# Optimization experiments

Hardware: AMD Instinct MI355X
Metric: run time of the kernel (lower is better)

## Reference

```python
import jax, jax.numpy as jnp
import numpy as np

N, K, C = 128, 64, 64

def _w(key, shape, scale):
    return (jax.random.normal(key, shape, dtype=jnp.float32) * scale)

def setup_inputs() -> dict:
    key = jax.random.key(0)
    ks = jax.random.split(key, 20)
    s1 = 1.0 / np.sqrt(C)
    s2 = 1.0 / np.sqrt(2 * C)
    inp = {
        "x": jax.random.normal(ks[0], (N, K, C), dtype=jnp.float32),
        "W_lin": _w(ks[1], (C, C), s1), "b_lin": jnp.zeros((C,), jnp.float32),
        # unary_passing: Linear(C,C) -> tanh -> Linear(C,C)
        "Wu1": _w(ks[2], (C, C), s1), "bu1": jnp.zeros((C,), jnp.float32),
        "Wu2": _w(ks[3], (C, C), s1), "bu2": jnp.zeros((C,), jnp.float32),
        # unary_gate: Linear(C,C) -> tanh -> Linear(C,C) -> sigmoid
        "Wug1": _w(ks[4], (C, C), s1), "bug1": jnp.zeros((C,), jnp.float32),
        "Wug2": _w(ks[5], (C, C), s1), "bug2": jnp.zeros((C,), jnp.float32),
        # binary_passing: Linear(2C,C) -> tanh -> Linear(C,C)
        "Wb1": _w(ks[6], (2 * C, C), s2), "bb1": jnp.zeros((C,), jnp.float32),
        "Wb2": _w(ks[7], (C, C), s1), "bb2": jnp.zeros((C,), jnp.float32),
        # binary_gate: Linear(2C,C) -> tanh -> Linear(C,C) -> sigmoid
        "Wbg1": _w(ks[8], (2 * C, C), s2), "bbg1": jnp.zeros((C,), jnp.float32),
        "Wbg2": _w(ks[9], (C, C), s1), "bbg2": jnp.zeros((C,), jnp.float32),
        "t": 0,  # time scalar, ignored by IgnoreLinear base layer
    }
    return inp


def reference(x, W_lin, b_lin, Wu1, bu1, Wu2, bu2, Wug1, bug1, Wug2, bug2,
              Wb1, bb1, Wb2, bb2, Wbg1, bbg1, Wbg2, bbg2, t):
    # base linear map (IgnoreLinear: ignores t)
    h = x @ W_lin + b_lin                          # (N, K, C)
    n, k, c = h.shape
    # unary message with gate
    um = jnp.tanh(h @ Wu1 + bu1) @ Wu2 + bu2
    ug = jax.nn.sigmoid(jnp.tanh(h @ Wug1 + bug1) @ Wug2 + bug2)
    um = um * ug                                   # (N, K, C)
    # all-pairs broadcast-concat: hm[n,i,j] = [h[n,j], h[n,i]]
    hm = jnp.concatenate([
        jnp.broadcast_to(h[:, None, :, :], (n, k, k, c)),
        jnp.broadcast_to(h[:, :, None, :], (n, k, k, c)),
    ], axis=3)                                     # (N, K, K, 2C)
    bm = jnp.tanh(hm @ Wb1 + bb1) @ Wb2 + bb2      # (N, K, K, C)
    bg = jax.nn.sigmoid(jnp.tanh(hm @ Wbg1 + bbg1) @ Wbg2 + bbg2)
    # sum over axis 1 (includes diagonal, as in original), normalize by K-1
    bm = jnp.sum(bm * bg, axis=1) / jnp.float32(k - 1)  # (N, K, C)
    return um + bm
```

## Files before the change

### kernel.cpp

```cpp
#include <hip/hip_runtime.h>

#define WST 72

typedef __attribute__((ext_vector_type(4))) float    f32x4;
typedef __attribute__((ext_vector_type(2))) float    f32x2;
typedef __attribute__((ext_vector_type(8))) _Float16 f16x8;
typedef __attribute__((ext_vector_type(2))) _Float16 f16x2;

__device__ __forceinline__ float rcp_f(float x) { return __builtin_amdgcn_rcpf(x); }
__device__ __forceinline__ float fast_sigmoid(float x) {
    return rcp_f(1.0f + __expf(-x));
}
__device__ __forceinline__ float tanh_exp(float x) {
    return 1.0f - 2.0f * rcp_f(__expf(2.0f * x) + 1.0f);
}

__device__ __forceinline__ void stage512(const float* __restrict__ W,
                                         _Float16* Wt, int tid) {
#pragma unroll
    for (int i = 0; i < 8; ++i) {
        int idx = tid + i * 512;
        int k = idx >> 6, c = idx & 63;
        Wt[c * WST + k] = (_Float16)W[idx];
    }
}

__device__ __forceinline__ void gemm2(const _Float16* Act, int arow, int qd,
                                      const _Float16* Wt, int colb,
                                      f32x4 acc[2]) {
    f16x8 a0 = *(const f16x8*)(Act + arow * WST + qd * 8);
    f16x8 a1 = *(const f16x8*)(Act + arow * WST + 32 + qd * 8);
#pragma unroll
    for (int cc = 0; cc < 2; ++cc) {
        const _Float16* wr = Wt + (colb + cc * 16) * WST + qd * 8;
        f16x8 b0 = *(const f16x8*)(wr);
        f16x8 b1 = *(const f16x8*)(wr + 32);
        acc[cc] = __builtin_amdgcn_mfma_f32_16x16x32_f16(a0, b0, acc[cc], 0, 0, 0);
        acc[cc] = __builtin_amdgcn_mfma_f32_16x16x32_f16(a1, b1, acc[cc], 0, 0, 0);
    }
}

__global__ __launch_bounds__(512, 2) void fused_all_kernel(
    const float* __restrict__ x,
    const float* __restrict__ W_lin, const float* __restrict__ b_lin,
    const float* __restrict__ Wu1,  const float* __restrict__ bu1,
    const float* __restrict__ Wu2,  const float* __restrict__ bu2,
    const float* __restrict__ Wug1, const float* __restrict__ bug1,
    const float* __restrict__ Wug2, const float* __restrict__ bug2,
    const float* __restrict__ Wb1,  const float* __restrict__ bb1,
    const float* __restrict__ Wb2,  const float* __restrict__ bb2,
    const float* __restrict__ Wbg1, const float* __restrict__ bbg1,
    const float* __restrict__ Wbg2, const float* __restrict__ bbg2,
    float* __restrict__ out)
{
    __shared__ __align__(16) char smem[113664];
    _Float16* Wt0  = (_Float16*)(smem);
    _Float16* Wt1  = (_Float16*)(smem + 9216);
    _Float16* Ax   = (_Float16*)(smem + 18432);
    _Float16* Ah   = (_Float16*)(smem + 27648);
    _Float16* Au   = (_Float16*)(smem + 36864);
    _Float16* Agg  = (_Float16*)(smem + 46080);
    float*    EQb  = (float*)(smem + 55296);
    float*    EQgb = (float*)(smem + 71680);
    float*    EPm  = (float*)(smem + 88064);
    float*    EPgm = (float*)(smem + 96768);
    float*    um32 = (float*)(smem + 105472);
    float*    Red  = (float*)(smem);

    int tid = threadIdx.x, w = tid >> 6, l = tid & 63;
    int qd = l >> 4, l16 = l & 15;
    int n = blockIdx.x >> 1, jsel = blockIdx.x & 1;

    int rw = w & 3, ch = w >> 2;
    int arow = rw * 16 + l16;
    int colb = ch * 32 + l16;
    int crow = rw * 16 + qd * 4;
    bool mine = (rw >> 1) == jsel;
    int lr0 = (rw & 1) * 16 + qd * 4;

    f32x4 acc[2];

#pragma unroll
    for (int i = 0; i < 4; ++i) {
        int e = tid * 2 + i * 1024;
        f32x2 v = *(const f32x2*)(x + (size_t)n * 4096 + e);
        f16x2 p; p[0] = (_Float16)v[0]; p[1] = (_Float16)v[1];
        *(f16x2*)(Ax + (e >> 6) * WST + (e & 63)) = p;
    }
    stage512(W_lin, Wt0, tid);
    __syncthreads();

#pragma unroll
    for (int cc = 0; cc < 2; ++cc) {
        float bv = b_lin[colb + cc * 16];
        acc[cc] = (f32x4){bv, bv, bv, bv};
    }
    gemm2(Ax, arow, qd, Wt0, colb, acc);
#pragma unroll
    for (int cc = 0; cc < 2; ++cc)
#pragma unroll
        for (int r = 0; r < 4; ++r)
            Ah[(crow + r) * WST + colb + cc * 16] = (_Float16)acc[cc][r];
    stage512(Wb1, Wt1, tid);
    __syncthreads();

#pragma unroll
    for (int cc = 0; cc < 2; ++cc) {
        float bv = bb1[colb + cc * 16];
        acc[cc] = (f32x4){bv, bv, bv, bv};
    }
    gemm2(Ah, arow, qd, Wt1, colb, acc);
    if (mine) {
#pragma unroll
        for (int cc = 0; cc < 2; ++cc)
#pragma unroll
            for (int r = 0; r < 4; ++r)
                EPm[(lr0 + r) * 68 + colb + cc * 16] = __expf(2.0f * acc[cc][r]);
    }
    stage512(Wb1 + 4096, Wt0, tid);
    __syncthreads();

    acc[0] = (f32x4){0.f, 0.f, 0.f, 0.f};
    acc[1] = (f32x4){0.f, 0.f, 0.f, 0.f};
    gemm2(Ah, arow, qd, Wt0, colb, acc);
#pragma unroll
    for (int cc = 0; cc < 2; ++cc)
#pragma unroll
        for (int r = 0; r < 4; ++r)
            EQb[(crow + r) * 64 + colb + cc * 16] = __expf(2.0f * acc[cc][r]);
    stage512(Wbg1, Wt1, tid);
    __syncthreads();

#pragma unroll
    for (int cc = 0; cc < 2; ++cc) {
        float bv = bbg1[colb + cc * 16];
        acc[cc] = (f32x4){bv, bv, bv, bv};
    }
    gemm2(Ah, arow, qd, Wt1, colb, acc);
    if (mine) {
#pragma unroll
        for (int cc = 0; cc < 2; ++cc)
#pragma unroll
            for (int r = 0; r < 4; ++r)
                EPgm[(lr0 + r) * 68 + colb + cc * 16] = __expf(2.0f * acc[cc][r]);
    }
    stage512(Wbg1 + 4096, Wt0, tid);
    __syncthreads();

    acc[0] = (f32x4){0.f, 0.f, 0.f, 0.f};
    acc[1] = (f32x4){0.f, 0.f, 0.f, 0.f};
    gemm2(Ah, arow, qd, Wt0, colb, acc);
#pragma unroll
    for (int cc = 0; cc < 2; ++cc)
#pragma unroll
        for (int r = 0; r < 4; ++r)
            EQgb[(crow + r) * 64 + colb + cc * 16] = __expf(2.0f * acc[cc][r]);
    stage512(Wu1, Wt1, tid);
    __syncthreads();

#pragma unroll
    for (int cc = 0; cc < 2; ++cc) {
        float bv = bu1[colb + cc * 16];
        acc[cc] = (f32x4){bv, bv, bv, bv};
    }
    gemm2(Ah, arow, qd, Wt1, colb, acc);
#pragma unroll
    for (int cc = 0; cc < 2; ++cc)
#pragma unroll
        for (int r = 0; r < 4; ++r)
            Au[(crow + r) * WST + colb + cc * 16] = (_Float16)tanh_exp(acc[cc][r]);
    stage512(Wug1, Wt0, tid);
    __syncthreads();

#pragma unroll
    for (int cc = 0; cc < 2; ++cc) {
        float bv = bug1[colb + cc * 16];
        acc[cc] = (f32x4){bv, bv, bv, bv};
    }
    gemm2(Ah, arow, qd, Wt0, colb, acc);
#pragma unroll
    for (int cc = 0; cc < 2; ++cc)
#pragma unroll
        for (int r = 0; r < 4; ++r)
            Agg[(crow + r) * WST + colb + cc * 16] = (_Float16)tanh_exp(acc[cc][r]);
    stage512(Wu2, Wt1, tid);
    __syncthreads();

    f32x4 uacc[2];
#pragma unroll
    for (int cc = 0; cc < 2; ++cc) {
        float bv = bu2[colb + cc * 16];
        uacc[cc] = (f32x4){bv, bv, bv, bv};
    }
    gemm2(Au, arow, qd, Wt1, colb, uacc);
    stage512(Wug2, Wt0, tid);
    __syncthreads();

#pragma unroll
    for (int cc = 0; cc < 2; ++cc) {
        float bv = bug2[colb + cc * 16];
        acc[cc] = (f32x4){bv, bv, bv, bv};
    }
    gemm2(Agg, arow, qd, Wt0, colb, acc);
    if (mine) {
#pragma unroll
        for (int cc = 0; cc < 2; ++cc)
#pragma unroll
            for (int r = 0; r < 4; ++r)
                um32[(lr0 + r) * 64 + colb + cc * 16] =
                    uacc[cc][r] * fast_sigmoid(acc[cc][r]);
    }
    stage512(Wb2, Wt1, tid);
    stage512(Wbg2, Au, tid);
    __syncthreads();

    int jgrp = w >> 2, iw = w & 3;

    f16x8 bwm[4][2], bwg[4][2];
#pragma unroll
    for (int cc = 0; cc < 4; ++cc)
#pragma unroll
        for (int kk = 0; kk < 2; ++kk) {
            bwm[cc][kk] = *(const f16x8*)(Wt1 + (cc * 16 + l16) * WST + kk * 32 + qd * 8);
            bwg[cc][kk] = *(const f16x8*)(Au  + (cc * 16 + l16) * WST + kk * 32 + qd * 8);
        }
    float bim[4], big[4];
#pragma unroll
    for (int cc = 0; cc < 4; ++cc) {
        bim[cc] = bb2[cc * 16 + l16];
        big[cc] = bbg2[cc * 16 + l16];
    }

    const float* pr  = EPm  + (jgrp * 16 + l16) * 68;
    const float* pgr = EPgm + (jgrp * 16 + l16) * 68;
    f32x4 pm[4], pg[4];
    pm[0] = *(const f32x4*)(pr + qd * 8);
    pm[1] = *(const f32x4*)(pr + qd * 8 + 4);
    pm[2] = *(const f32x4*)(pr + 32 + qd * 8);
    pm[3] = *(const f32x4*)(pr + 32 + qd * 8 + 4);
    pg[0] = *(const f32x4*)(pgr + qd * 8);
    pg[1] = *(const f32x4*)(pgr + qd * 8 + 4);
    pg[2] = *(const f32x4*)(pgr + 32 + qd * 8);
    pg[3] = *(const f32x4*)(pgr + 32 + qd * 8 + 4);

    f32x4 bacc[4];
#pragma unroll
    for (int cc = 0; cc < 4; ++cc) bacc[cc] = (f32x4){0.f, 0.f, 0.f, 0.f};

    for (int ii = iw * 16; ii < iw * 16 + 16; ++ii) {
        const float* qm = EQb  + ii * 64;
        const float* qg = EQgb + ii * 64;
        f16x8 am[2], ag[2];
#pragma unroll
        for (int kk = 0; kk < 2; ++kk) {
            int cb = kk * 32 + qd * 8;
            f32x4 qa = *(const f32x4*)(qm + cb);
            f32x4 qb = *(const f32x4*)(qm + cb + 4);
            f32x4 ha = *(const f32x4*)(qg + cb);
            f32x4 hb = *(const f32x4*)(qg + cb + 4);
#pragma unroll
            for (int t = 0; t < 4; ++t) {
                am[kk][t]     = (_Float16)(1.0f - 2.0f * rcp_f(__builtin_fmaf(pm[kk*2][t],   qa[t], 1.0f)));
                am[kk][t + 4] = (_Float16)(1.0f - 2.0f * rcp_f(__builtin_fmaf(pm[kk*2+1][t], qb[t], 1.0f)));
                ag[kk][t]     = (_Float16)(1.0f - 2.0f * rcp_f(__builtin_fmaf(pg[kk*2][t],   ha[t], 1.0f)));
                ag[kk][t + 4] = (_Float16)(1.0f - 2.0f * rcp_f(__builtin_fmaf(pg[kk*2+1][t], hb[t], 1.0f)));
            }
        }
#pragma unroll
        for (int cc = 0; cc < 4; ++cc) {
            f32x4 d = {bim[cc], bim[cc], bim[cc], bim[cc]};
            d = __builtin_amdgcn_mfma_f32_16x16x32_f16(am[0], bwm[cc][0], d, 0, 0, 0);
            d = __builtin_amdgcn_mfma_f32_16x16x32_f16(am[1], bwm[cc][1], d, 0, 0, 0);
            f32x4 e = {big[cc], big[cc], big[cc], big[cc]};
            e = __builtin_amdgcn_mfma_f32_16x16x32_f16(ag[0], bwg[cc][0], e, 0, 0, 0);
            e = __builtin_amdgcn_mfma_f32_16x16x32_f16(ag[1], bwg[cc][1], e, 0, 0, 0);
#pragma unroll
            for (int r = 0; r < 4; ++r)
                bacc[cc][r] += d[r] * fast_sigmoid(e[r]);
        }
    }

    __syncthreads();
#pragma unroll
    for (int cc = 0; cc < 4; ++cc)
#pragma unroll
        for (int r = 0; r < 4; ++r)
            Red[(jgrp * 4 + iw) * 1024 + (qd * 4 + r) * 64 + cc * 16 + l16] = bacc[cc][r];
    __syncthreads();

    {
        int e = tid * 4;
        int lr = e >> 6, col = e & 63;
        int g = lr >> 4, rr = lr & 15;
        f32x4 s = {0.f, 0.f, 0.f, 0.f};
#pragma unroll
        for (int w2 = 0; w2 < 4; ++w2)
            s += *(const f32x4*)(Red + (g * 4 + w2) * 1024 + rr * 64 + col);
        f32x4 u = *(const f32x4*)(um32 + lr * 64 + col);
        f32x4 o;
#pragma unroll
        for (int t = 0; t < 4; ++t)
            o[t] = u[t] + s[t] * (1.0f / 63.0f);
        *(f32x4*)(out + (size_t)n * 4096 + (size_t)(jsel * 32 + lr) * 64 + col) = o;
    }
}

extern "C" void kernel_launch(void* const* d_in, const int* in_sizes, int n_in,
                              void* d_out, int out_size, void* d_ws, size_t ws_size,
                              hipStream_t stream)
{
    (void)in_sizes; (void)n_in; (void)out_size; (void)d_ws; (void)ws_size;
    const float* x     = (const float*)d_in[0];
    const float* W_lin = (const float*)d_in[1];
    const float* b_lin = (const float*)d_in[2];
    const float* Wu1   = (const float*)d_in[3];
    const float* bu1   = (const float*)d_in[4];
    const float* Wu2   = (const float*)d_in[5];
    const float* bu2   = (const float*)d_in[6];
    const float* Wug1  = (const float*)d_in[7];
    const float* bug1  = (const float*)d_in[8];
    const float* Wug2  = (const float*)d_in[9];
    const float* bug2  = (const float*)d_in[10];
    const float* Wb1   = (const float*)d_in[11];
    const float* bb1   = (const float*)d_in[12];
    const float* Wb2   = (const float*)d_in[13];
    const float* bb2   = (const float*)d_in[14];
    const float* Wbg1  = (const float*)d_in[15];
    const float* bbg1  = (const float*)d_in[16];
    const float* Wbg2  = (const float*)d_in[17];
    const float* bbg2  = (const float*)d_in[18];

    hipLaunchKernelGGL(fused_all_kernel, dim3(256), dim3(512), 0, stream,
        x, W_lin, b_lin, Wu1, bu1, Wu2, bu2, Wug1, bug1, Wug2, bug2,
        Wb1, bb1, Wb2, bb2, Wbg1, bbg1, Wbg2, bbg2,
        (float*)d_out);
}
```

Baseline: 118.7 us.

## Split each batch into four blocks, fold tanh/sigmoid constants into weights

The grid doubles to four blocks per batch element, each producing 16 output rows. Shared memory drops to about 78 KB and launch bounds now allow 4 blocks per CU, aiming for higher occupancy and more parallelism. The tanh affine terms are folded into the second-layer weights and biases by scaling W by -2 and 2*log2e and using column sums, so the inner loop computes reciprocals without the 1-2x step and uses exp2. Paired reciprocals, packed RTZ half conversion, and per-iteration LDS weight loads replace register-held weights. In exchange, the small prologue GEMMs are recomputed across the four blocks, and fp16 rounding of the scaled weights may shift accuracy slightly.

```diff
diff --git a/kernel.cpp b/kernel.cpp
--- a/kernel.cpp
+++ b/kernel.cpp
@@ -1,28 +1,43 @@
 #include <hip/hip_runtime.h>
 
 #define WST 72
+#define LOG2E 1.44269504f
 
 typedef __attribute__((ext_vector_type(4))) float    f32x4;
 typedef __attribute__((ext_vector_type(2))) float    f32x2;
 typedef __attribute__((ext_vector_type(8))) _Float16 f16x8;
 typedef __attribute__((ext_vector_type(2))) _Float16 f16x2;
+typedef __attribute__((ext_vector_type(2))) __fp16   fp16x2_raw;
+
+union U8 { f16x8 v; f16x2 h[4]; };
 
 __device__ __forceinline__ float rcp_f(float x) { return __builtin_amdgcn_rcpf(x); }
+__device__ __forceinline__ float exp2_f(float x) { return __builtin_amdgcn_exp2f(x); }
 __device__ __forceinline__ float fast_sigmoid(float x) {
     return rcp_f(1.0f + __expf(-x));
 }
 __device__ __forceinline__ float tanh_exp(float x) {
     return 1.0f - 2.0f * rcp_f(__expf(2.0f * x) + 1.0f);
 }
-
-__device__ __forceinline__ void stage512(const float* __restrict__ W,
-                                         _Float16* Wt, int tid) {
+__device__ __forceinline__ f16x2 pkrtz(float a, float b) {
+    fp16x2_raw r = __builtin_amdgcn_cvt_pkrtz(a, b);
+    return __builtin_bit_cast(f16x2, r);
+}
+
+__device__ __forceinline__ void stage_w(const float* __restrict__ W, _Float16* Wt,
+                                        int tid, float scale, float* csbuf) {
+    float v[8];
+#pragma unroll
+    for (int i = 0; i < 8; ++i) v[i] = W[tid + i * 512];
+    float cs = 0.0f;
 #pragma unroll
     for (int i = 0; i < 8; ++i) {
         int idx = tid + i * 512;
-        int k = idx >> 6, c = idx & 63;
-        Wt[c * WST + k] = (_Float16)W[idx];
-    }
+        _Float16 hv = (_Float16)(v[i] * scale);
+        Wt[(idx & 63) * WST + (idx >> 6)] = hv;
+        cs += (float)hv;
+    }
+    if (csbuf) csbuf[(tid >> 6) * 64 + (tid & 63)] = cs;
 }
 
 __device__ __forceinline__ void gemm2(const _Float16* Act, int arow, int qd,
@@ -40,7 +55,7 @@
     }
 }
 
-__global__ __launch_bounds__(512, 2) void fused_all_kernel(
+__global__ __launch_bounds__(512, 4) void fused_all_kernel(
     const float* __restrict__ x,
     const float* __restrict__ W_lin, const float* __restrict__ b_lin,
     const float* __restrict__ Wu1,  const float* __restrict__ bu1,
@@ -53,30 +68,32 @@
     const float* __restrict__ Wbg2, const float* __restrict__ bbg2,
     float* __restrict__ out)
 {
-    __shared__ __align__(16) char smem[113664];
-    _Float16* Wt0  = (_Float16*)(smem);
-    _Float16* Wt1  = (_Float16*)(smem + 9216);
-    _Float16* Ax   = (_Float16*)(smem + 18432);
-    _Float16* Ah   = (_Float16*)(smem + 27648);
-    _Float16* Au   = (_Float16*)(smem + 36864);
-    _Float16* Agg  = (_Float16*)(smem + 46080);
-    float*    EQb  = (float*)(smem + 55296);
-    float*    EQgb = (float*)(smem + 71680);
-    float*    EPm  = (float*)(smem + 88064);
-    float*    EPgm = (float*)(smem + 96768);
-    float*    um32 = (float*)(smem + 105472);
-    float*    Red  = (float*)(smem);
+    __shared__ __align__(16) char smem[78336];
+    _Float16* A  = (_Float16*)(smem);
+    _Float16* B  = (_Float16*)(smem + 9216);
+    _Float16* C  = (_Float16*)(smem + 18432);
+    _Float16* SH = (_Float16*)(smem + 27648);
+    float*    um  = (float*)(smem + 27648);
+    float*    csm = (float*)(smem + 31744);
+    float*    csg = (float*)(smem + 33792);
+    float*    EQb  = (float*)(smem + 36864);
+    float*    EQgb = (float*)(smem + 53248);
+    float*    EPm  = (float*)(smem + 69632);
+    float*    EPgm = (float*)(smem + 73984);
+    float*    Red  = (float*)(smem + 36864);
 
     int tid = threadIdx.x, w = tid >> 6, l = tid & 63;
     int qd = l >> 4, l16 = l & 15;
-    int n = blockIdx.x >> 1, jsel = blockIdx.x & 1;
+    int n = blockIdx.x >> 2, jq = blockIdx.x & 3;
 
     int rw = w & 3, ch = w >> 2;
     int arow = rw * 16 + l16;
     int colb = ch * 32 + l16;
     int crow = rw * 16 + qd * 4;
-    bool mine = (rw >> 1) == jsel;
-    int lr0 = (rw & 1) * 16 + qd * 4;
+
+    int wp = w & 1;
+    int colb16 = wp * 32 + l16;
+    bool g01 = (w < 2), g23 = (w >= 2) && (w < 4);
 
     f32x4 acc[2];
 
@@ -85,9 +102,9 @@
         int e = tid * 2 + i * 1024;
         f32x2 v = *(const f32x2*)(x + (size_t)n * 4096 + e);
         f16x2 p; p[0] = (_Float16)v[0]; p[1] = (_Float16)v[1];
-        *(f16x2*)(Ax + (e >> 6) * WST + (e & 63)) = p;
-    }
-    stage512(W_lin, Wt0, tid);
+        *(f16x2*)(A + (e >> 6) * WST + (e & 63)) = p;
+    }
+    stage_w(W_lin, B, tid, 1.0f, nullptr);
     __syncthreads();
 
 #pragma unroll
@@ -95,144 +112,152 @@
         float bv = b_lin[colb + cc * 16];
         acc[cc] = (f32x4){bv, bv, bv, bv};
     }
-    gemm2(Ax, arow, qd, Wt0, colb, acc);
+    gemm2(A, arow, qd, B, colb, acc);
 #pragma unroll
     for (int cc = 0; cc < 2; ++cc)
 #pragma unroll
         for (int r = 0; r < 4; ++r)
-            Ah[(crow + r) * WST + colb + cc * 16] = (_Float16)acc[cc][r];
-    stage512(Wb1, Wt1, tid);
-    __syncthreads();
-
-#pragma unroll
-    for (int cc = 0; cc < 2; ++cc) {
-        float bv = bb1[colb + cc * 16];
-        acc[cc] = (f32x4){bv, bv, bv, bv};
-    }
-    gemm2(Ah, arow, qd, Wt1, colb, acc);
-    if (mine) {
-#pragma unroll
-        for (int cc = 0; cc < 2; ++cc)
-#pragma unroll
-            for (int r = 0; r < 4; ++r)
-                EPm[(lr0 + r) * 68 + colb + cc * 16] = __expf(2.0f * acc[cc][r]);
-    }
-    stage512(Wb1 + 4096, Wt0, tid);
+            SH[(crow + r) * WST + colb + cc * 16] = (_Float16)acc[cc][r];
+    stage_w(Wb1 + 4096, C, tid, 1.0f, nullptr);
     __syncthreads();
 
     acc[0] = (f32x4){0.f, 0.f, 0.f, 0.f};
     acc[1] = (f32x4){0.f, 0.f, 0.f, 0.f};
-    gemm2(Ah, arow, qd, Wt0, colb, acc);
+    gemm2(SH, arow, qd, C, colb, acc);
 #pragma unroll
     for (int cc = 0; cc < 2; ++cc)
 #pragma unroll
         for (int r = 0; r < 4; ++r)
             EQb[(crow + r) * 64 + colb + cc * 16] = __expf(2.0f * acc[cc][r]);
-    stage512(Wbg1, Wt1, tid);
-    __syncthreads();
-
-#pragma unroll
-    for (int cc = 0; cc < 2; ++cc) {
-        float bv = bbg1[colb + cc * 16];
-        acc[cc] = (f32x4){bv, bv, bv, bv};
-    }
-    gemm2(Ah, arow, qd, Wt1, colb, acc);
-    if (mine) {
-#pragma unroll
-        for (int cc = 0; cc < 2; ++cc)
-#pragma unroll
-            for (int r = 0; r < 4; ++r)
-                EPgm[(lr0 + r) * 68 + colb + cc * 16] = __expf(2.0f * acc[cc][r]);
-    }
-    stage512(Wbg1 + 4096, Wt0, tid);
+    stage_w(Wb1, A, tid, 1.0f, nullptr);
+    __syncthreads();
+
+    if (g01) {
+#pragma unroll
+        for (int cc = 0; cc < 2; ++cc) {
+            float bv = bb1[colb16 + cc * 16];
+            acc[cc] = (f32x4){bv, bv, bv, bv};
+        }
+        gemm2(SH, jq * 16 + l16, qd, A, colb16, acc);
+#pragma unroll
+        for (int cc = 0; cc < 2; ++cc)
+#pragma unroll
+            for (int r = 0; r < 4; ++r)
+                EPm[(qd * 4 + r) * 68 + colb16 + cc * 16] = __expf(2.0f * acc[cc][r]);
+    }
+    stage_w(Wbg1 + 4096, C, tid, 1.0f, nullptr);
     __syncthreads();
 
     acc[0] = (f32x4){0.f, 0.f, 0.f, 0.f};
     acc[1] = (f32x4){0.f, 0.f, 0.f, 0.f};
-    gemm2(Ah, arow, qd, Wt0, colb, acc);
+    gemm2(SH, arow, qd, C, colb, acc);
 #pragma unroll
     for (int cc = 0; cc < 2; ++cc)
 #pragma unroll
         for (int r = 0; r < 4; ++r)
             EQgb[(crow + r) * 64 + colb + cc * 16] = __expf(2.0f * acc[cc][r]);
-    stage512(Wu1, Wt1, tid);
-    __syncthreads();
-
-#pragma unroll
-    for (int cc = 0; cc < 2; ++cc) {
-        float bv = bu1[colb + cc * 16];
-        acc[cc] = (f32x4){bv, bv, bv, bv};
-    }
-    gemm2(Ah, arow, qd, Wt1, colb, acc);
-#pragma unroll
-    for (int cc = 0; cc < 2; ++cc)
-#pragma unroll
-        for (int r = 0; r < 4; ++r)
-            Au[(crow + r) * WST + colb + cc * 16] = (_Float16)tanh_exp(acc[cc][r]);
-    stage512(Wug1, Wt0, tid);
-    __syncthreads();
-
-#pragma unroll
-    for (int cc = 0; cc < 2; ++cc) {
-        float bv = bug1[colb + cc * 16];
-        acc[cc] = (f32x4){bv, bv, bv, bv};
-    }
-    gemm2(Ah, arow, qd, Wt0, colb, acc);
-#pragma unroll
-    for (int cc = 0; cc < 2; ++cc)
-#pragma unroll
-        for (int r = 0; r < 4; ++r)
-            Agg[(crow + r) * WST + colb + cc * 16] = (_Float16)tanh_exp(acc[cc][r]);
-    stage512(Wu2, Wt1, tid);
-    __syncthreads();
-
-    f32x4 uacc[2];
-#pragma unroll
-    for (int cc = 0; cc < 2; ++cc) {
-        float bv = bu2[colb + cc * 16];
-        uacc[cc] = (f32x4){bv, bv, bv, bv};
-    }
-    gemm2(Au, arow, qd, Wt1, colb, uacc);
-    stage512(Wug2, Wt0, tid);
-    __syncthreads();
-
-#pragma unroll
-    for (int cc = 0; cc < 2; ++cc) {
-        float bv = bug2[colb + cc * 16];
-        acc[cc] = (f32x4){bv, bv, bv, bv};
-    }
-    gemm2(Agg, arow, qd, Wt0, colb, acc);
-    if (mine) {
-#pragma unroll
-        for (int cc = 0; cc < 2; ++cc)
-#pragma unroll
-            for (int r = 0; r < 4; ++r)
-                um32[(lr0 + r) * 64 + colb + cc * 16] =
-                    uacc[cc][r] * fast_sigmoid(acc[cc][r]);
-    }
-    stage512(Wb2, Wt1, tid);
-    stage512(Wbg2, Au, tid);
-    __syncthreads();
-
-    int jgrp = w >> 2, iw = w & 3;
-
-    f16x8 bwm[4][2], bwg[4][2];
-#pragma unroll
-    for (int cc = 0; cc < 4; ++cc)
-#pragma unroll
-        for (int kk = 0; kk < 2; ++kk) {
-            bwm[cc][kk] = *(const f16x8*)(Wt1 + (cc * 16 + l16) * WST + kk * 32 + qd * 8);
-            bwg[cc][kk] = *(const f16x8*)(Au  + (cc * 16 + l16) * WST + kk * 32 + qd * 8);
-        }
+    stage_w(Wbg1, A, tid, 1.0f, nullptr);
+    __syncthreads();
+
+    if (g23) {
+#pragma unroll
+        for (int cc = 0; cc < 2; ++cc) {
+            float bv = bbg1[colb16 + cc * 16];
+            acc[cc] = (f32x4){bv, bv, bv, bv};
+        }
+        gemm2(SH, jq * 16 + l16, qd, A, colb16, acc);
+#pragma unroll
+        for (int cc = 0; cc < 2; ++cc)
+#pragma unroll
+            for (int r = 0; r < 4; ++r)
+                EPgm[(qd * 4 + r) * 68 + colb16 + cc * 16] = __expf(2.0f * acc[cc][r]);
+    }
+    stage_w(Wu1, C, tid, 1.0f, nullptr);
+    __syncthreads();
+
+    if (g01) {
+#pragma unroll
+        for (int cc = 0; cc < 2; ++cc) {
+            float bv = bu1[colb16 + cc * 16];
+            acc[cc] = (f32x4){bv, bv, bv, bv};
+        }
+        gemm2(SH, jq * 16 + l16, qd, C, colb16, acc);
+#pragma unroll
+        for (int cc = 0; cc < 2; ++cc)
+#pragma unroll
+            for (int r = 0; r < 4; ++r)
+                B[(qd * 4 + r) * WST + colb16 + cc * 16] = (_Float16)tanh_exp(acc[cc][r]);
+    }
+    stage_w(Wug1, A, tid, 1.0f, nullptr);
+    __syncthreads();
+
+    if (g23) {
+#pragma unroll
+        for (int cc = 0; cc < 2; ++cc) {
+            float bv = bug1[colb16 + cc * 16];
+            acc[cc] = (f32x4){bv, bv, bv, bv};
+        }
+        gemm2(SH, jq * 16 + l16, qd, A, colb16, acc);
+#pragma unroll
+        for (int cc = 0; cc < 2; ++cc)
+#pragma unroll
+            for (int r = 0; r < 4; ++r)
+                B[(16 + qd * 4 + r) * WST + colb16 + cc * 16] = (_Float16)tanh_exp(acc[cc][r]);
+    }
+    stage_w(Wu2, C, tid, 1.0f, nullptr);
+    __syncthreads();
+
+    f32x4 ua[2];
+    if (g01) {
+#pragma unroll
+        for (int cc = 0; cc < 2; ++cc) {
+            float bv = bu2[colb16 + cc * 16];
+            ua[cc] = (f32x4){bv, bv, bv, bv};
+        }
+        gemm2(B, l16, qd, C, colb16, ua);
+    }
+    stage_w(Wug2, A, tid, 1.0f, nullptr);
+    __syncthreads();
+
+    f32x4 ga[2];
+    if (g01) {
+#pragma unroll
+        for (int cc = 0; cc < 2; ++cc) {
+            float bv = bug2[colb16 + cc * 16];
+            ga[cc] = (f32x4){bv, bv, bv, bv};
+        }
+        gemm2(B, 16 + l16, qd, A, colb16, ga);
+    }
+    stage_w(Wb2, C, tid, -2.0f, csm);
+    __syncthreads();
+
+    if (g01) {
+#pragma unroll
+        for (int cc = 0; cc < 2; ++cc)
+#pragma unroll
+            for (int r = 0; r < 4; ++r)
+                um[(qd * 4 + r) * 64 + colb16 + cc * 16] =
+                    ua[cc][r] * fast_sigmoid(ga[cc][r]);
+    }
+    stage_w(Wbg2, A, tid, 2.0f * LOG2E, csg);
+    __syncthreads();
+
     float bim[4], big[4];
 #pragma unroll
     for (int cc = 0; cc < 4; ++cc) {
-        bim[cc] = bb2[cc * 16 + l16];
-        big[cc] = bbg2[cc * 16 + l16];
-    }
-
-    const float* pr  = EPm  + (jgrp * 16 + l16) * 68;
-    const float* pgr = EPgm + (jgrp * 16 + l16) * 68;
+        int c = cc * 16 + l16;
+        float sm = 0.0f, sg = 0.0f;
+#pragma unroll
+        for (int m = 0; m < 8; ++m) {
+            sm += csm[m * 64 + c];
+            sg += csg[m * 64 + c];
+        }
+        bim[cc] = bb2[c] - 0.5f * sm;
+        big[cc] = -LOG2E * bbg2[c] - 0.5f * sg;
+    }
+
+    const float* pr  = EPm  + l16 * 68;
+    const float* pgr = EPgm + l16 * 68;
     f32x4 pm[4], pg[4];
     pm[0] = *(const f32x4*)(pr + qd * 8);
     pm[1] = *(const f32x4*)(pr + qd * 8 + 4);
@@ -247,10 +272,12 @@
 #pragma unroll
     for (int cc = 0; cc < 4; ++cc) bacc[cc] = (f32x4){0.f, 0.f, 0.f, 0.f};
 
-    for (int ii = iw * 16; ii < iw * 16 + 16; ++ii) {
+#pragma unroll 2
+    for (int ii = w * 8; ii < w * 8 + 8; ++ii) {
+        asm volatile("" ::: "memory");
         const float* qm = EQb  + ii * 64;
         const float* qg = EQgb + ii * 64;
-        f16x8 am[2], ag[2];
+        U8 am[2], ag[2];
 #pragma unroll
         for (int kk = 0; kk < 2; ++kk) {
             int cb = kk * 32 + qd * 8;
@@ -259,24 +286,49 @@
             f32x4 ha = *(const f32x4*)(qg + cb);
             f32x4 hb = *(const f32x4*)(qg + cb + 4);
 #pragma unroll
-            for (int t = 0; t < 4; ++t) {
-                am[kk][t]     = (_Float16)(1.0f - 2.0f * rcp_f(__builtin_fmaf(pm[kk*2][t],   qa[t], 1.0f)));
-                am[kk][t + 4] = (_Float16)(1.0f - 2.0f * rcp_f(__builtin_fmaf(pm[kk*2+1][t], qb[t], 1.0f)));
-                ag[kk][t]     = (_Float16)(1.0f - 2.0f * rcp_f(__builtin_fmaf(pg[kk*2][t],   ha[t], 1.0f)));
-                ag[kk][t + 4] = (_Float16)(1.0f - 2.0f * rcp_f(__builtin_fmaf(pg[kk*2+1][t], hb[t], 1.0f)));
+            for (int t = 0; t < 2; ++t) {
+                float a0 = __builtin_fmaf(pm[kk*2][2*t],   qa[2*t],   1.0f);
+                float a1 = __builtin_fmaf(pm[kk*2][2*t+1], qa[2*t+1], 1.0f);
+                float ri = rcp_f(a0 * a1);
+                am[kk].h[t]     = pkrtz(ri * a1, ri * a0);
+                float b0f = __builtin_fmaf(pm[kk*2+1][2*t],   qb[2*t],   1.0f);
+                float b1f = __builtin_fmaf(pm[kk*2+1][2*t+1], qb[2*t+1], 1.0f);
+                float rj = rcp_f(b0f * b1f);
+                am[kk].h[2 + t] = pkrtz(rj * b1f, rj * b0f);
+                float c0 = __builtin_fmaf(pg[kk*2][2*t],   ha[2*t],   1.0f);
+                float c1 = __builtin_fmaf(pg[kk*2][2*t+1], ha[2*t+1], 1.0f);
+                float rk = rcp_f(c0 * c1);
+                ag[kk].h[t]     = pkrtz(rk * c1, rk * c0);
+                float d0 = __builtin_fmaf(pg[kk*2+1][2*t],   hb[2*t],   1.0f);
+                float d1 = __builtin_fmaf(pg[kk*2+1][2*t+1], hb[2*t+1], 1.0f);
+                float rl = rcp_f(d0 * d1);
+                ag[kk].h[2 + t] = pkrtz(rl * d1, rl * d0);
             }
         }
 #pragma unroll
         for (int cc = 0; cc < 4; ++cc) {
+            const _Float16* wm = C + (cc * 16 + l16) * WST + qd * 8;
+            const _Float16* wg = A + (cc * 16 + l16) * WST + qd * 8;
+            f16x8 bm0 = *(const f16x8*)(wm);
+            f16x8 bm1 = *(const f16x8*)(wm + 32);
+            f16x8 bg0 = *(const f16x8*)(wg);
+            f16x8 bg1 = *(const f16x8*)(wg + 32);
             f32x4 d = {bim[cc], bim[cc], bim[cc], bim[cc]};
-            d = __builtin_amdgcn_mfma_f32_16x16x32_f16(am[0], bwm[cc][0], d, 0, 0, 0);
-            d = __builtin_amdgcn_mfma_f32_16x16x32_f16(am[1], bwm[cc][1], d, 0, 0, 0);
+            d = __builtin_amdgcn_mfma_f32_16x16x32_f16(am[0].v, bm0, d, 0, 0, 0);
+            d = __builtin_amdgcn_mfma_f32_16x16x32_f16(am[1].v, bm1, d, 0, 0, 0);
             f32x4 e = {big[cc], big[cc], big[cc], big[cc]};
-            e = __builtin_amdgcn_mfma_f32_16x16x32_f16(ag[0], bwg[cc][0], e, 0, 0, 0);
-            e = __builtin_amdgcn_mfma_f32_16x16x32_f16(ag[1], bwg[cc][1], e, 0, 0, 0);
-#pragma unroll
-            for (int r = 0; r < 4; ++r)
-                bacc[cc][r] += d[r] * fast_sigmoid(e[r]);
+            e = __builtin_amdgcn_mfma_f32_16x16x32_f16(ag[0].v, bg0, e, 0, 0, 0);
+            e = __builtin_amdgcn_mfma_f32_16x16x32_f16(ag[1].v, bg1, e, 0, 0, 0);
+            float v0 = exp2_f(e[0]), v1 = exp2_f(e[1]);
+            float u0 = 1.0f + v0, u1 = 1.0f + v1;
+            float r01 = rcp_f(u0 * u1);
+            bacc[cc][0] = __builtin_fmaf(d[0] * u1, r01, bacc[cc][0]);
+            bacc[cc][1] = __builtin_fmaf(d[1] * u0, r01, bacc[cc][1]);
+            float v2 = exp2_f(e[2]), v3 = exp2_f(e[3]);
+            float u2 = 1.0f + v2, u3 = 1.0f + v3;
+            float r23 = rcp_f(u2 * u3);
+            bacc[cc][2] = __builtin_fmaf(d[2] * u3, r23, bacc[cc][2]);
+            bacc[cc][3] = __builtin_fmaf(d[3] * u2, r23, bacc[cc][3]);
         }
     }
 
@@ -285,23 +337,21 @@
     for (int cc = 0; cc < 4; ++cc)
 #pragma unroll
         for (int r = 0; r < 4; ++r)
-            Red[(jgrp * 4 + iw) * 1024 + (qd * 4 + r) * 64 + cc * 16 + l16] = bacc[cc][r];
+            Red[w * 1024 + (qd * 4 + r) * 64 + cc * 16 + l16] = bacc[cc][r];
     __syncthreads();
 
     {
-        int e = tid * 4;
+        int e = tid * 2;
         int lr = e >> 6, col = e & 63;
-        int g = lr >> 4, rr = lr & 15;
-        f32x4 s = {0.f, 0.f, 0.f, 0.f};
-#pragma unroll
-        for (int w2 = 0; w2 < 4; ++w2)
-            s += *(const f32x4*)(Red + (g * 4 + w2) * 1024 + rr * 64 + col);
-        f32x4 u = *(const f32x4*)(um32 + lr * 64 + col);
-        f32x4 o;
-#pragma unroll
-        for (int t = 0; t < 4; ++t)
-            o[t] = u[t] + s[t] * (1.0f / 63.0f);
-        *(f32x4*)(out + (size_t)n * 4096 + (size_t)(jsel * 32 + lr) * 64 + col) = o;
+        f32x2 s = {0.f, 0.f};
+#pragma unroll
+        for (int p = 0; p < 8; ++p)
+            s += *(const f32x2*)(Red + p * 1024 + lr * 64 + col);
+        f32x2 u = *(const f32x2*)(um + lr * 64 + col);
+        f32x2 o;
+        o[0] = u[0] + s[0] * (1.0f / 63.0f);
+        o[1] = u[1] + s[1] * (1.0f / 63.0f);
+        *(f32x2*)(out + (size_t)n * 4096 + (size_t)(jq * 16 + lr) * 64 + col) = o;
     }
 }
 
@@ -330,7 +380,7 @@
     const float* Wbg2  = (const float*)d_in[17];
     const float* bbg2  = (const float*)d_in[18];
 
-    hipLaunchKernelGGL(fused_all_kernel, dim3(256), dim3(512), 0, stream,
+    hipLaunchKernelGGL(fused_all_kernel, dim3(512), dim3(512), 0, stream,
         x, W_lin, b_lin, Wu1, bu1, Wu2, bu2, Wug1, bug1, Wug2, bug2,
         Wb1, bb1, Wb2, bb2, Wbg1, bbg1, Wbg2, bbg2,
         (float*)d_out);
```

Result: no change. 118.7 us (+0.0%).
